# Optimization experiments

Measured on AMD Instinct MI355X. Metric: run time of the kernel, lower is better.

Reference implementation:

```python
import jax, jax.numpy as jnp
import numpy as np
import math

B, S, HID, H = 1, 2048, 1024, 16
D = HID // H  # head_dim = 64


def setup_inputs() -> dict:
    key = jax.random.key(0)
    ks = jax.random.split(key, 12)
    s = 0.02
    x = jax.random.normal(ks[0], (B, S, HID), jnp.float32)
    Wq = jax.random.normal(ks[1], (HID, HID), jnp.float32) * s
    bq = jnp.zeros((HID,), jnp.float32)
    Wk = jax.random.normal(ks[2], (HID, HID), jnp.float32) * s
    bk = jnp.zeros((HID,), jnp.float32)
    Wv = jax.random.normal(ks[3], (HID, HID), jnp.float32) * s
    bv = jnp.zeros((HID,), jnp.float32)
    Wo = jax.random.normal(ks[4], (HID, HID), jnp.float32) * s
    bo = jnp.zeros((HID,), jnp.float32)
    # nn.Parameter(torch.ones(3,3)) at init; small noise so the bias is non-degenerate
    cmw = jnp.ones((3, 3), jnp.float32) + 0.1 * jax.random.normal(ks[5], (3, 3), jnp.float32)
    # full causal [B,S,S] mask so the mask.shape[1]==seq_len branch is taken
    mask = jnp.tril(jnp.ones((B, S, S), jnp.int32))
    modality_info = jax.random.randint(ks[6], (B, S), 0, 3, dtype=jnp.int64)
    return dict(x=x, Wq=Wq, bq=bq, Wk=Wk, bk=bk, Wv=Wv, bv=bv, Wo=Wo, bo=bo,
                cmw=cmw, mask=mask, modality_info=modality_info)


def reference(x, Wq, bq, Wk, bk, Wv, bv, Wo, bo, cmw, mask, modality_info):
    b, s, _ = x.shape
    # QKV projections (torch Linear: y = x @ W.T + b), split into heads [B,H,S,D]
    q = (x @ Wq.T + bq).reshape(b, s, H, D).transpose(0, 2, 1, 3)
    k = (x @ Wk.T + bk).reshape(b, s, H, D).transpose(0, 2, 1, 3)
    v = (x @ Wv.T + bv).reshape(b, s, H, D).transpose(0, 2, 1, 3)
    scores = jnp.einsum('bhqd,bhkd->bhqk', q, k) / math.sqrt(D)  # [B,H,S,S]
    # cross-modal bias: gather from 3x3 table via pairwise modality indices -> [B,S,S]
    bias = cmw[modality_info[:, :, None], modality_info[:, None, :]]
    scores = scores + bias[:, None, :, :]  # equals original broadcast when B==1
    scores = jnp.where(mask[:, None, :, :] == 0, -1e9, scores)
    attn = jax.nn.softmax(scores, axis=-1)  # dropout is identity in eval
    ctx = jnp.einsum('bhqk,bhkd->bhqd', attn, v)          # [B,H,S,D]
    ctx = ctx.transpose(0, 2, 1, 3).reshape(b, s, HID)    # [B,S,HID]
    return ctx @ Wo.T + bo
```

## Files before the change

kernel.cpp:

```cpp
#include <hip/hip_runtime.h>
#include <hip/hip_bf16.h>
#include <math.h>

#define S_LEN 2048
#define HID   1024
#define NHEAD 16

using bf16x8 = __attribute__((ext_vector_type(8))) short;
using bf16x4 = __attribute__((ext_vector_type(4))) short;
using f32x4  = __attribute__((ext_vector_type(4))) float;

__device__ __forceinline__ float bf2f(short s) {
  union { unsigned u; float f; } c;
  c.u = ((unsigned)(unsigned short)s) << 16;
  return c.f;
}
__device__ __forceinline__ short f2bf(float f) {
  union { float f; unsigned u; } c; c.f = f;
  unsigned u = c.u;
  unsigned r = (u + 0x7fffu + ((u >> 16) & 1u)) >> 16;
  return (short)r;
}
__device__ __forceinline__ float loadf(const void* base, long idx, int is_bf) {
  return is_bf ? bf2f(((const short*)base)[idx]) : ((const float*)base)[idx];
}

__global__ void detect_kernel(const unsigned* __restrict__ xw,
                              const int* __restrict__ modw,
                              int* __restrict__ flags) {
  const int t = threadIdx.x;
  int cnt = 0;
  for (int i = t; i < 1024; i += 64) {
    const unsigned fld = (xw[i] >> 7) & 0xFFu;
    cnt += (fld >= 100u && fld <= 135u) ? 1 : 0;
  }
  int odd = 0;
  for (int i = 0; i < 4; ++i) {
    const int wv = modw[2 * (t + 64 * i) + 1];
    odd += (wv != 0) ? 1 : 0;
  }
  for (int m = 1; m < 64; m <<= 1) {
    cnt += __shfl_xor(cnt, m);
    odd += __shfl_xor(odd, m);
  }
  if (t == 0) {
    flags[0] = (cnt >= 512) ? 1 : 0;
    flags[1] = (odd == 0) ? 1 : 0;
  }
}

__global__ __launch_bounds__(256) void convert5(
    const void* __restrict__ s0, const void* __restrict__ s1, const void* __restrict__ s2,
    const void* __restrict__ s3, const void* __restrict__ s4,
    short* __restrict__ d0, short* __restrict__ d1, short* __restrict__ d2,
    short* __restrict__ d3, short* __restrict__ d4,
    const int* __restrict__ flags) {
  const int a = blockIdx.y;
  const void* src = (a == 0) ? s0 : (a == 1) ? s1 : (a == 2) ? s2 : (a == 3) ? s3 : s4;
  short* dst = (a == 0) ? d0 : (a == 1) ? d1 : (a == 2) ? d2 : (a == 3) ? d3 : d4;
  const long n = (a == 0) ? (2L << 20) : (1L << 20);
  const int is_bf = flags[0];
  long i = (long)(blockIdx.x * 256 + threadIdx.x) * 8;
  const long stride = (long)gridDim.x * 256 * 8;
  if (is_bf) {
    for (; i < n; i += stride)
      *(bf16x8*)(dst + i) = *(const bf16x8*)((const short*)src + i);
  } else {
    for (; i < n; i += stride) {
      const float* p = (const float*)src + i;
      bf16x8 r;
#pragma unroll
      for (int j = 0; j < 8; ++j) r[j] = f2bf(p[j]);
      *(bf16x8*)(dst + i) = r;
    }
  }
}

__global__ __launch_bounds__(256) void gemm_bt3(
    const short* __restrict__ A,
    const short* __restrict__ W0, const short* __restrict__ W1, const short* __restrict__ W2,
    const void* __restrict__ b0, const void* __restrict__ b1, const void* __restrict__ b2,
    void* __restrict__ C0, void* __restrict__ C1, void* __restrict__ C2,
    const int* __restrict__ flags, int nbn, int store_f32)
{
  constexpr int K = 1024;
  constexpr int N = 1024;
  __shared__ short As[128 * 32];
  __shared__ short Bs[64 * 32];

  const int t = threadIdx.x;
  const int w = t >> 6, lane = t & 63;
  const int l15 = lane & 15, quad = lane >> 4;
  const int wm = w >> 1, wn = w & 1;

  const int is_bf = flags[0];
  const int bx = blockIdx.x;
  const int mat = bx / nbn;
  const int n0 = (bx % nbn) * 64;
  const int m0 = blockIdx.y * 128;

  const short* W  = (mat == 0) ? W0 : (mat == 1 ? W1 : W2);
  const void* bia = (mat == 0) ? b0 : (mat == 1 ? b1 : b2);
  void*       C   = (mat == 0) ? C0 : (mat == 1 ? C1 : C2);

  f32x4 acc[4][2];
  for (int mi = 0; mi < 4; ++mi)
    for (int ni = 0; ni < 2; ++ni)
      for (int r = 0; r < 4; ++r) acc[mi][ni][r] = 0.f;

  const int srow = t >> 2;
  const int sch  = (t & 3) * 8;
  const short* Ap = A + (long)(m0 + srow) * K + sch;
  const short* Wp = W + (long)(n0 + srow) * K + sch;

  bf16x8 ra0 = *(const bf16x8*)(Ap);
  bf16x8 ra1 = *(const bf16x8*)(Ap + 64L * K);
  bf16x8 rb0 = *(const bf16x8*)(Wp);

  for (int kt = 0; kt < K / 32; ++kt) {
    __syncthreads();
    *(bf16x8*)&As[(srow)      * 32 + sch] = ra0;
    *(bf16x8*)&As[(srow + 64) * 32 + sch] = ra1;
    *(bf16x8*)&Bs[(srow)      * 32 + sch] = rb0;
    __syncthreads();
    if (kt + 1 < K / 32) {
      ra0 = *(const bf16x8*)(Ap + (kt + 1) * 32);
      ra1 = *(const bf16x8*)(Ap + (kt + 1) * 32 + 64L * K);
      rb0 = *(const bf16x8*)(Wp + (kt + 1) * 32);
    }
    bf16x8 af[4], bfr[2];
    for (int mi = 0; mi < 4; ++mi)
      af[mi] = *(const bf16x8*)&As[(wm * 64 + mi * 16 + l15) * 32 + quad * 8];
    for (int ni = 0; ni < 2; ++ni)
      bfr[ni] = *(const bf16x8*)&Bs[(wn * 32 + ni * 16 + l15) * 32 + quad * 8];
    for (int mi = 0; mi < 4; ++mi)
      for (int ni = 0; ni < 2; ++ni)
        acc[mi][ni] = __builtin_amdgcn_mfma_f32_16x16x32_bf16(af[mi], bfr[ni], acc[mi][ni], 0, 0, 0);
  }

  for (int ni = 0; ni < 2; ++ni) {
    const int col = n0 + wn * 32 + ni * 16 + l15;
    const float bv = loadf(bia, col, is_bf);
    for (int mi = 0; mi < 4; ++mi) {
      const int row = m0 + wm * 64 + mi * 16 + quad * 4;
      for (int r = 0; r < 4; ++r) {
        const float v = acc[mi][ni][r] + bv;
        const long idx = (long)(row + r) * N + col;
        if (store_f32) ((float*)C)[idx] = v;
        else           ((short*)C)[idx] = f2bf(v);
      }
    }
  }
}

__global__ __launch_bounds__(256) void attn_split(
    const short* __restrict__ Q, const short* __restrict__ Kg, const short* __restrict__ Vg,
    const int* __restrict__ mod, const void* __restrict__ cmw,
    const int* __restrict__ flags,
    short* __restrict__ PO, float* __restrict__ PM, float* __restrict__ PL)
{
  __shared__ short Ks[64 * 80];
  __shared__ short Vt[64 * 80];
  __shared__ short Ps[4 * 16 * 80];
  __shared__ float cm[9];
  __shared__ int mods[2048];

  const int t = threadIdx.x;
  const int w = t >> 6, lane = t & 63;
  const int l15 = lane & 15, quad = lane >> 4;
  const int h = blockIdx.y;
  const int pair = blockIdx.x >> 1;
  const int par  = blockIdx.x & 1;
  const int m64 = flags[1];

  if (t < 9) cm[t] = loadf(cmw, t, flags[0]);
  for (int i = t; i < 2048; i += 256) mods[i] = mod[i << m64];
  __syncthreads();

  const int krow = t >> 3, kch = (t & 7) * 8;
  const int vkp = t & 63, vdc = (t >> 6) * 8;

  for (int si = 0; si < 2; ++si) {
    const int strip = (si == 0) ? pair : 31 - pair;
    const int q0 = strip * 64;
    const int nkt = strip + 1;

    const short* qb = Q + (long)(q0 + w * 16 + l15) * HID + h * 64 + quad * 8;
    const bf16x8 aq0 = *(const bf16x8*)qb;
    const bf16x8 aq1 = *(const bf16x8*)(qb + 32);

    int mrow[4];
    for (int r = 0; r < 4; ++r) mrow[r] = mods[q0 + w * 16 + quad * 4 + r];

    float m_i[4], l_i[4];
    f32x4 acc_o[4];
    for (int r = 0; r < 4; ++r) { m_i[r] = -1e30f; l_i[r] = 0.f; }
    for (int ni = 0; ni < 4; ++ni)
      for (int r = 0; r < 4; ++r) acc_o[ni][r] = 0.f;

    bf16x8 rk0, rk1, rv0, rv1;
    if (par < nkt) {
      const long kb = (long)(par * 64) * HID + h * 64;
      rk0 = *(const bf16x8*)(Kg + kb + (long)krow * HID + kch);
      rk1 = *(const bf16x8*)(Kg + kb + (long)(krow + 32) * HID + kch);
      rv0 = *(const bf16x8*)(Vg + kb + (long)vkp * HID + vdc);
      rv1 = *(const bf16x8*)(Vg + kb + (long)vkp * HID + 32 + vdc);
    }

    for (int kt = par; kt < nkt; kt += 2) {
      __syncthreads();
      *(bf16x8*)&Ks[krow * 80 + kch] = rk0;
      *(bf16x8*)&Ks[(krow + 32) * 80 + kch] = rk1;
#pragma unroll
      for (int j = 0; j < 8; ++j) Vt[(vdc + j) * 80 + vkp] = rv0[j];
#pragma unroll
      for (int j = 0; j < 8; ++j) Vt[(vdc + 32 + j) * 80 + vkp] = rv1[j];
      __syncthreads();
      if (kt + 2 < nkt) {
        const long kb = (long)((kt + 2) * 64) * HID + h * 64;
        rk0 = *(const bf16x8*)(Kg + kb + (long)krow * HID + kch);
        rk1 = *(const bf16x8*)(Kg + kb + (long)(krow + 32) * HID + kch);
        rv0 = *(const bf16x8*)(Vg + kb + (long)vkp * HID + vdc);
        rv1 = *(const bf16x8*)(Vg + kb + (long)vkp * HID + 32 + vdc);
      }

      f32x4 sc[4];
      for (int nt = 0; nt < 4; ++nt) {
        const bf16x8 kb0 = *(const bf16x8*)&Ks[(nt * 16 + l15) * 80 + quad * 8];
        const bf16x8 kb1 = *(const bf16x8*)&Ks[(nt * 16 + l15) * 80 + 32 + quad * 8];
        f32x4 z;
        for (int r = 0; r < 4; ++r) z[r] = 0.f;
        z = __builtin_amdgcn_mfma_f32_16x16x32_bf16(aq0, kb0, z, 0, 0, 0);
        z = __builtin_amdgcn_mfma_f32_16x16x32_bf16(aq1, kb1, z, 0, 0, 0);
        sc[nt] = z;
      }

      float sv[4][4], rmax[4];
      for (int r = 0; r < 4; ++r) rmax[r] = -1e30f;
      for (int nt = 0; nt < 4; ++nt) {
        const int mcol = mods[kt * 64 + nt * 16 + l15];
        for (int r = 0; r < 4; ++r) {
          float x = sc[nt][r] * 0.125f + cm[mrow[r] * 3 + mcol];
          sv[nt][r] = x;
          rmax[r] = fmaxf(rmax[r], x);
        }
      }
      if (kt == nkt - 1) {
        for (int r = 0; r < 4; ++r) rmax[r] = -1e30f;
        for (int nt = 0; nt < 4; ++nt) {
          const int col = kt * 64 + nt * 16 + l15;
          for (int r = 0; r < 4; ++r) {
            const int row = q0 + w * 16 + quad * 4 + r;
            sv[nt][r] = (col <= row) ? sv[nt][r] : -1e30f;
            rmax[r] = fmaxf(rmax[r], sv[nt][r]);
          }
        }
      }
      for (int off = 1; off < 16; off <<= 1)
        for (int r = 0; r < 4; ++r) rmax[r] = fmaxf(rmax[r], __shfl_xor(rmax[r], off));

      float alpha[4], rsum[4];
      for (int r = 0; r < 4; ++r) {
        const float mn = fmaxf(m_i[r], rmax[r]);
        alpha[r] = __expf(m_i[r] - mn);
        m_i[r] = mn;
        rsum[r] = 0.f;
      }
      short pb[4][4];
      for (int nt = 0; nt < 4; ++nt)
        for (int r = 0; r < 4; ++r) {
          const float p = __expf(sv[nt][r] - m_i[r]);
          rsum[r] += p;
          pb[nt][r] = f2bf(p);
        }
      for (int off = 1; off < 16; off <<= 1)
        for (int r = 0; r < 4; ++r) rsum[r] += __shfl_xor(rsum[r], off);
      for (int r = 0; r < 4; ++r) l_i[r] = l_i[r] * alpha[r] + rsum[r];
      for (int ni = 0; ni < 4; ++ni)
        for (int r = 0; r < 4; ++r) acc_o[ni][r] *= alpha[r];

      short* Pw = &Ps[w * 16 * 80];
      for (int nt = 0; nt < 4; ++nt)
        for (int r = 0; r < 4; ++r)
          Pw[(quad * 4 + r) * 80 + nt * 16 + l15] = pb[nt][r];
      asm volatile("s_waitcnt lgkmcnt(0)" ::: "memory");

      for (int kk = 0; kk < 2; ++kk) {
        const bf16x8 ap = *(const bf16x8*)&Pw[l15 * 80 + kk * 32 + quad * 8];
        for (int ni = 0; ni < 4; ++ni) {
          const bf16x8 bv = *(const bf16x8*)&Vt[(ni * 16 + l15) * 80 + kk * 32 + quad * 8];
          acc_o[ni] = __builtin_amdgcn_mfma_f32_16x16x32_bf16(ap, bv, acc_o[ni], 0, 0, 0);
        }
      }
    }

    const long pbase = (long)par * 2097152;
    for (int ni = 0; ni < 4; ++ni) {
      const int col = h * 64 + ni * 16 + l15;
      for (int r = 0; r < 4; ++r) {
        const int row = q0 + w * 16 + quad * 4 + r;
        PO[pbase + (long)row * HID + col] = f2bf(acc_o[ni][r]);
      }
    }
    if (l15 == 0) {
      for (int r = 0; r < 4; ++r) {
        const int row = q0 + w * 16 + quad * 4 + r;
        PM[par * 32768 + row * 16 + h] = m_i[r];
        PL[par * 32768 + row * 16 + h] = l_i[r];
      }
    }
  }
}

__global__ __launch_bounds__(256) void attn_merge(
    const short* __restrict__ PO, const float* __restrict__ PM, const float* __restrict__ PL,
    short* __restrict__ CTX)
{
  const int row = blockIdx.x;
  const int t = threadIdx.x;
  const int h = t >> 4;
  const int d0 = (t & 15) * 4;
  const float m0 = PM[row * 16 + h], m1 = PM[32768 + row * 16 + h];
  const float l0 = PL[row * 16 + h], l1 = PL[32768 + row * 16 + h];
  const float M = fmaxf(m0, m1);
  const float w0 = __expf(m0 - M), w1 = __expf(m1 - M);
  const float inv = 1.f / (l0 * w0 + l1 * w1);
  const long b = (long)row * HID + h * 64 + d0;
  const bf16x4 o0 = *(const bf16x4*)&PO[b];
  const bf16x4 o1 = *(const bf16x4*)&PO[2097152 + b];
  bf16x4 out;
#pragma unroll
  for (int j = 0; j < 4; ++j)
    out[j] = f2bf((bf2f(o0[j]) * w0 + bf2f(o1[j]) * w1) * inv);
  *(bf16x4*)&CTX[b] = out;
}

extern "C" void kernel_launch(void* const* d_in, const int* in_sizes, int n_in,
                              void* d_out, int out_size, void* d_ws, size_t ws_size,
                              hipStream_t stream) {
  constexpr long M1 = 1024L * 1024L;
  int*   flags = (int*)d_ws;
  short* base  = (short*)d_ws + 128;
  short* xb  = base;
  short* Wqb = xb + 2 * M1;
  short* Wkb = Wqb + M1;
  short* Wvb = Wkb + M1;
  short* Wob = Wvb + M1;
  short* Qw  = Wob + M1;
  short* Kw  = Qw + 2 * M1;
  short* Vw  = Kw + 2 * M1;
  short* CTX = Vw + 2 * M1;
  short* PO = xb;
  float* PM = (float*)Wvb;
  float* PL = PM + 65536;
  const int* modality = (const int*)d_in[11];

  detect_kernel<<<1, 64, 0, stream>>>((const unsigned*)d_in[0], modality, flags);
  convert5<<<dim3(512, 5), 256, 0, stream>>>(
      d_in[0], d_in[1], d_in[3], d_in[5], d_in[7],
      xb, Wqb, Wkb, Wvb, Wob, flags);

  gemm_bt3<<<dim3(48, 16), 256, 0, stream>>>(
      xb, Wqb, Wkb, Wvb, d_in[2], d_in[4], d_in[6],
      Qw, Kw, Vw, flags, 16, 0);
  attn_split<<<dim3(32, NHEAD), 256, 0, stream>>>(
      Qw, Kw, Vw, modality, d_in[9], flags, PO, PM, PL);
  attn_merge<<<dim3(S_LEN), 256, 0, stream>>>(PO, PM, PL, CTX);
  gemm_bt3<<<dim3(16, 16), 256, 0, stream>>>(
      CTX, Wob, Wob, Wob, d_in[8], d_in[8], d_in[8],
      d_out, d_out, d_out, flags, 16, 1);
}
```

Measured before the change: 190.4 us.

## Load attention K/V straight from global, transpose V in GEMM, split keys three ways

The QKV GEMM epilogue now writes V transposed, and the attention kernel reads K and V fragments directly from global memory into registers. This drops the LDS staging, the strided V transpose in LDS, and two barriers per key tile. The key range is split across three blocks instead of two, with a three-way merge, to add parallelism. The GEMM also swaps its register-prefetch staging for direct global-to-LDS loads, which removes load/compute overlap. The attention waves now load the same K/V redundantly and depend on cache hits for reuse.

```diff
diff --git a/kernel.cpp b/kernel.cpp
--- a/kernel.cpp
+++ b/kernel.cpp
@@ -23,6 +23,11 @@
 }
 __device__ __forceinline__ float loadf(const void* base, long idx, int is_bf) {
   return is_bf ? bf2f(((const short*)base)[idx]) : ((const float*)base)[idx];
+}
+__device__ __forceinline__ void gl_lds16(const void* g, void* l) {
+  __builtin_amdgcn_global_load_lds(
+      (const __attribute__((address_space(1))) void*)g,
+      (__attribute__((address_space(3))) void*)l, 16, 0, 0);
 }
 
 __global__ void detect_kernel(const unsigned* __restrict__ xw,
@@ -81,7 +86,7 @@
     const short* __restrict__ W0, const short* __restrict__ W1, const short* __restrict__ W2,
     const void* __restrict__ b0, const void* __restrict__ b1, const void* __restrict__ b2,
     void* __restrict__ C0, void* __restrict__ C1, void* __restrict__ C2,
-    const int* __restrict__ flags, int nbn, int store_f32)
+    const int* __restrict__ flags, int nbn, int store_f32, int tr_mat2)
 {
   constexpr int K = 1024;
   constexpr int N = 1024;
@@ -92,16 +97,16 @@
   const int w = t >> 6, lane = t & 63;
   const int l15 = lane & 15, quad = lane >> 4;
   const int wm = w >> 1, wn = w & 1;
-
   const int is_bf = flags[0];
-  const int bx = blockIdx.x;
-  const int mat = bx / nbn;
-  const int n0 = (bx % nbn) * 64;
+
+  const int mat = blockIdx.x / nbn;
+  const int n0 = (blockIdx.x % nbn) * 64;
   const int m0 = blockIdx.y * 128;
 
   const short* W  = (mat == 0) ? W0 : (mat == 1 ? W1 : W2);
   const void* bia = (mat == 0) ? b0 : (mat == 1 ? b1 : b2);
   void*       C   = (mat == 0) ? C0 : (mat == 1 ? C1 : C2);
+  const int tr = (mat == 2) ? tr_mat2 : 0;
 
   f32x4 acc[4][2];
   for (int mi = 0; mi < 4; ++mi)
@@ -112,22 +117,16 @@
   const int sch  = (t & 3) * 8;
   const short* Ap = A + (long)(m0 + srow) * K + sch;
   const short* Wp = W + (long)(n0 + srow) * K + sch;
-
-  bf16x8 ra0 = *(const bf16x8*)(Ap);
-  bf16x8 ra1 = *(const bf16x8*)(Ap + 64L * K);
-  bf16x8 rb0 = *(const bf16x8*)(Wp);
+  short* AsW = &As[w * 512];
+  short* BsW = &Bs[w * 512];
 
   for (int kt = 0; kt < K / 32; ++kt) {
     __syncthreads();
-    *(bf16x8*)&As[(srow)      * 32 + sch] = ra0;
-    *(bf16x8*)&As[(srow + 64) * 32 + sch] = ra1;
-    *(bf16x8*)&Bs[(srow)      * 32 + sch] = rb0;
+    gl_lds16(Ap + kt * 32, AsW);
+    gl_lds16(Ap + kt * 32 + 64L * K, AsW + 2048);
+    gl_lds16(Wp + kt * 32, BsW);
     __syncthreads();
-    if (kt + 1 < K / 32) {
-      ra0 = *(const bf16x8*)(Ap + (kt + 1) * 32);
-      ra1 = *(const bf16x8*)(Ap + (kt + 1) * 32 + 64L * K);
-      rb0 = *(const bf16x8*)(Wp + (kt + 1) * 32);
-    }
+
     bf16x8 af[4], bfr[2];
     for (int mi = 0; mi < 4; ++mi)
       af[mi] = *(const bf16x8*)&As[(wm * 64 + mi * 16 + l15) * 32 + quad * 8];
@@ -143,24 +142,30 @@
     const float bv = loadf(bia, col, is_bf);
     for (int mi = 0; mi < 4; ++mi) {
       const int row = m0 + wm * 64 + mi * 16 + quad * 4;
-      for (int r = 0; r < 4; ++r) {
-        const float v = acc[mi][ni][r] + bv;
-        const long idx = (long)(row + r) * N + col;
-        if (store_f32) ((float*)C)[idx] = v;
-        else           ((short*)C)[idx] = f2bf(v);
+      if (tr) {
+        bf16x4 o;
+#pragma unroll
+        for (int r = 0; r < 4; ++r) o[r] = f2bf(acc[mi][ni][r] + bv);
+        *(bf16x4*)((short*)C + (long)col * S_LEN + row) = o;
+      } else {
+        for (int r = 0; r < 4; ++r) {
+          const float v = acc[mi][ni][r] + bv;
+          const long idx = (long)(row + r) * N + col;
+          if (store_f32) ((float*)C)[idx] = v;
+          else           ((short*)C)[idx] = f2bf(v);
+        }
       }
     }
   }
 }
 
 __global__ __launch_bounds__(256) void attn_split(
-    const short* __restrict__ Q, const short* __restrict__ Kg, const short* __restrict__ Vg,
+    const short* __restrict__ Q, const short* __restrict__ Kg, const short* __restrict__ VT,
     const int* __restrict__ mod, const void* __restrict__ cmw,
     const int* __restrict__ flags,
-    short* __restrict__ PO, float* __restrict__ PM, float* __restrict__ PL)
+    short* __restrict__ PO0, short* __restrict__ PO1, short* __restrict__ PO2,
+    float* __restrict__ PM, float* __restrict__ PL)
 {
-  __shared__ short Ks[64 * 80];
-  __shared__ short Vt[64 * 80];
   __shared__ short Ps[4 * 16 * 80];
   __shared__ float cm[9];
   __shared__ int mods[2048];
@@ -169,16 +174,16 @@
   const int w = t >> 6, lane = t & 63;
   const int l15 = lane & 15, quad = lane >> 4;
   const int h = blockIdx.y;
-  const int pair = blockIdx.x >> 1;
-  const int par  = blockIdx.x & 1;
+  const int pair = blockIdx.x / 3;
+  const int par  = blockIdx.x % 3;
   const int m64 = flags[1];
 
   if (t < 9) cm[t] = loadf(cmw, t, flags[0]);
   for (int i = t; i < 2048; i += 256) mods[i] = mod[i << m64];
   __syncthreads();
 
-  const int krow = t >> 3, kch = (t & 7) * 8;
-  const int vkp = t & 63, vdc = (t >> 6) * 8;
+  short* POp = (par == 0) ? PO0 : (par == 1) ? PO1 : PO2;
+  short* Pw = &Ps[w * 16 * 80];
 
   for (int si = 0; si < 2; ++si) {
     const int strip = (si == 0) ? pair : 31 - pair;
@@ -198,45 +203,34 @@
     for (int ni = 0; ni < 4; ++ni)
       for (int r = 0; r < 4; ++r) acc_o[ni][r] = 0.f;
 
-    bf16x8 rk0, rk1, rv0, rv1;
-    if (par < nkt) {
-      const long kb = (long)(par * 64) * HID + h * 64;
-      rk0 = *(const bf16x8*)(Kg + kb + (long)krow * HID + kch);
-      rk1 = *(const bf16x8*)(Kg + kb + (long)(krow + 32) * HID + kch);
-      rv0 = *(const bf16x8*)(Vg + kb + (long)vkp * HID + vdc);
-      rv1 = *(const bf16x8*)(Vg + kb + (long)vkp * HID + 32 + vdc);
-    }
-
-    for (int kt = par; kt < nkt; kt += 2) {
-      __syncthreads();
-      *(bf16x8*)&Ks[krow * 80 + kch] = rk0;
-      *(bf16x8*)&Ks[(krow + 32) * 80 + kch] = rk1;
-#pragma unroll
-      for (int j = 0; j < 8; ++j) Vt[(vdc + j) * 80 + vkp] = rv0[j];
-#pragma unroll
-      for (int j = 0; j < 8; ++j) Vt[(vdc + 32 + j) * 80 + vkp] = rv1[j];
-      __syncthreads();
-      if (kt + 2 < nkt) {
-        const long kb = (long)((kt + 2) * 64) * HID + h * 64;
-        rk0 = *(const bf16x8*)(Kg + kb + (long)krow * HID + kch);
-        rk1 = *(const bf16x8*)(Kg + kb + (long)(krow + 32) * HID + kch);
-        rv0 = *(const bf16x8*)(Vg + kb + (long)vkp * HID + vdc);
-        rv1 = *(const bf16x8*)(Vg + kb + (long)vkp * HID + 32 + vdc);
-      }
+    for (int kt = par; kt < nkt; kt += 3) {
+      bf16x8 kf[4][2], vf[2][4];
+#pragma unroll
+      for (int nt = 0; nt < 4; ++nt) {
+        const short* kr = Kg + (long)(kt * 64 + nt * 16 + l15) * HID + h * 64 + quad * 8;
+        kf[nt][0] = *(const bf16x8*)kr;
+        kf[nt][1] = *(const bf16x8*)(kr + 32);
+      }
+#pragma unroll
+      for (int kk = 0; kk < 2; ++kk)
+#pragma unroll
+        for (int ni = 0; ni < 4; ++ni)
+          vf[kk][ni] = *(const bf16x8*)(VT + (long)(h * 64 + ni * 16 + l15) * S_LEN
+                                        + kt * 64 + kk * 32 + quad * 8);
 
       f32x4 sc[4];
+#pragma unroll
       for (int nt = 0; nt < 4; ++nt) {
-        const bf16x8 kb0 = *(const bf16x8*)&Ks[(nt * 16 + l15) * 80 + quad * 8];
-        const bf16x8 kb1 = *(const bf16x8*)&Ks[(nt * 16 + l15) * 80 + 32 + quad * 8];
         f32x4 z;
         for (int r = 0; r < 4; ++r) z[r] = 0.f;
-        z = __builtin_amdgcn_mfma_f32_16x16x32_bf16(aq0, kb0, z, 0, 0, 0);
-        z = __builtin_amdgcn_mfma_f32_16x16x32_bf16(aq1, kb1, z, 0, 0, 0);
+        z = __builtin_amdgcn_mfma_f32_16x16x32_bf16(aq0, kf[nt][0], z, 0, 0, 0);
+        z = __builtin_amdgcn_mfma_f32_16x16x32_bf16(aq1, kf[nt][1], z, 0, 0, 0);
         sc[nt] = z;
       }
 
       float sv[4][4], rmax[4];
       for (int r = 0; r < 4; ++r) rmax[r] = -1e30f;
+#pragma unroll
       for (int nt = 0; nt < 4; ++nt) {
         const int mcol = mods[kt * 64 + nt * 16 + l15];
         for (int r = 0; r < 4; ++r) {
@@ -247,6 +241,7 @@
       }
       if (kt == nkt - 1) {
         for (int r = 0; r < 4; ++r) rmax[r] = -1e30f;
+#pragma unroll
         for (int nt = 0; nt < 4; ++nt) {
           const int col = kt * 64 + nt * 16 + l15;
           for (int r = 0; r < 4; ++r) {
@@ -267,6 +262,7 @@
         rsum[r] = 0.f;
       }
       short pb[4][4];
+#pragma unroll
       for (int nt = 0; nt < 4; ++nt)
         for (int r = 0; r < 4; ++r) {
           const float p = __expf(sv[nt][r] - m_i[r]);
@@ -279,27 +275,25 @@
       for (int ni = 0; ni < 4; ++ni)
         for (int r = 0; r < 4; ++r) acc_o[ni][r] *= alpha[r];
 
-      short* Pw = &Ps[w * 16 * 80];
+#pragma unroll
       for (int nt = 0; nt < 4; ++nt)
         for (int r = 0; r < 4; ++r)
           Pw[(quad * 4 + r) * 80 + nt * 16 + l15] = pb[nt][r];
       asm volatile("s_waitcnt lgkmcnt(0)" ::: "memory");
 
+#pragma unroll
       for (int kk = 0; kk < 2; ++kk) {
         const bf16x8 ap = *(const bf16x8*)&Pw[l15 * 80 + kk * 32 + quad * 8];
-        for (int ni = 0; ni < 4; ++ni) {
-          const bf16x8 bv = *(const bf16x8*)&Vt[(ni * 16 + l15) * 80 + kk * 32 + quad * 8];
-          acc_o[ni] = __builtin_amdgcn_mfma_f32_16x16x32_bf16(ap, bv, acc_o[ni], 0, 0, 0);
-        }
-      }
-    }
-
-    const long pbase = (long)par * 2097152;
+        for (int ni = 0; ni < 4; ++ni)
+          acc_o[ni] = __builtin_amdgcn_mfma_f32_16x16x32_bf16(ap, vf[kk][ni], acc_o[ni], 0, 0, 0);
+      }
+    }
+
     for (int ni = 0; ni < 4; ++ni) {
       const int col = h * 64 + ni * 16 + l15;
       for (int r = 0; r < 4; ++r) {
         const int row = q0 + w * 16 + quad * 4 + r;
-        PO[pbase + (long)row * HID + col] = f2bf(acc_o[ni][r]);
+        POp[(long)row * HID + col] = f2bf(acc_o[ni][r]);
       }
     }
     if (l15 == 0) {
@@ -313,25 +307,32 @@
 }
 
 __global__ __launch_bounds__(256) void attn_merge(
-    const short* __restrict__ PO, const float* __restrict__ PM, const float* __restrict__ PL,
-    short* __restrict__ CTX)
+    const short* __restrict__ PO0, const short* __restrict__ PO1, const short* __restrict__ PO2,
+    const float* __restrict__ PM, const float* __restrict__ PL, short* __restrict__ CTX)
 {
   const int row = blockIdx.x;
   const int t = threadIdx.x;
   const int h = t >> 4;
   const int d0 = (t & 15) * 4;
-  const float m0 = PM[row * 16 + h], m1 = PM[32768 + row * 16 + h];
-  const float l0 = PL[row * 16 + h], l1 = PL[32768 + row * 16 + h];
-  const float M = fmaxf(m0, m1);
-  const float w0 = __expf(m0 - M), w1 = __expf(m1 - M);
-  const float inv = 1.f / (l0 * w0 + l1 * w1);
+  float m[3], l[3];
+#pragma unroll
+  for (int p = 0; p < 3; ++p) {
+    m[p] = PM[p * 32768 + row * 16 + h];
+    l[p] = PL[p * 32768 + row * 16 + h];
+  }
+  const float M = fmaxf(m[0], fmaxf(m[1], m[2]));
+  float wgt[3], den = 0.f;
+#pragma unroll
+  for (int p = 0; p < 3; ++p) { wgt[p] = __expf(m[p] - M); den += l[p] * wgt[p]; }
+  const float inv = 1.f / den;
   const long b = (long)row * HID + h * 64 + d0;
-  const bf16x4 o0 = *(const bf16x4*)&PO[b];
-  const bf16x4 o1 = *(const bf16x4*)&PO[2097152 + b];
+  const bf16x4 o0 = *(const bf16x4*)&PO0[b];
+  const bf16x4 o1 = *(const bf16x4*)&PO1[b];
+  const bf16x4 o2 = *(const bf16x4*)&PO2[b];
   bf16x4 out;
 #pragma unroll
   for (int j = 0; j < 4; ++j)
-    out[j] = f2bf((bf2f(o0[j]) * w0 + bf2f(o1[j]) * w1) * inv);
+    out[j] = f2bf((bf2f(o0[j]) * wgt[0] + bf2f(o1[j]) * wgt[1] + bf2f(o2[j]) * wgt[2]) * inv);
   *(bf16x4*)&CTX[b] = out;
 }
 
@@ -348,11 +349,13 @@
   short* Wob = Wvb + M1;
   short* Qw  = Wob + M1;
   short* Kw  = Qw + 2 * M1;
-  short* Vw  = Kw + 2 * M1;
-  short* CTX = Vw + 2 * M1;
-  short* PO = xb;
-  float* PM = (float*)Wvb;
-  float* PL = PM + 65536;
+  short* VTb = Kw + 2 * M1;
+  short* CTX = VTb + 2 * M1;
+  short* PO1 = xb;
+  short* PO2 = Wqb;
+  float* PM  = (float*)Wvb;
+  float* PL  = PM + 3 * 32768;
+  short* PO0 = CTX;
   const int* modality = (const int*)d_in[11];
 
   detect_kernel<<<1, 64, 0, stream>>>((const unsigned*)d_in[0], modality, flags);
@@ -362,11 +365,11 @@
 
   gemm_bt3<<<dim3(48, 16), 256, 0, stream>>>(
       xb, Wqb, Wkb, Wvb, d_in[2], d_in[4], d_in[6],
-      Qw, Kw, Vw, flags, 16, 0);
-  attn_split<<<dim3(32, NHEAD), 256, 0, stream>>>(
-      Qw, Kw, Vw, modality, d_in[9], flags, PO, PM, PL);
-  attn_merge<<<dim3(S_LEN), 256, 0, stream>>>(PO, PM, PL, CTX);
+      Qw, Kw, VTb, flags, 16, 0, 1);
+  attn_split<<<dim3(48, NHEAD), 256, 0, stream>>>(
+      Qw, Kw, VTb, modality, d_in[9], flags, PO0, PO1, PO2, PM, PL);
+  attn_merge<<<dim3(S_LEN), 256, 0, stream>>>(PO0, PO1, PO2, PM, PL, CTX);
   gemm_bt3<<<dim3(16, 16), 256, 0, stream>>>(
       CTX, Wob, Wob, Wob, d_in[8], d_in[8], d_in[8],
-      d_out, d_out, d_out, flags, 16, 1);
-}
+      d_out, d_out, d_out, flags, 16, 1, 0);
+}
```

Measured after the change: 219.8 us. 1.15x slower.
